# Kernel optimization log

Measured on AMD Instinct MI355X. Metric: run time of the kernel, lower is better.

The kernel has to match this reference:

```python
import jax, jax.numpy as jnp
import numpy as np

# Module hyper-parameters (match init_kwargs)
WIN = 64        # windowSize -> N
REC = 128       # receptiveSize -> M
H = 8           # numHeads
D = 32          # headDim
DIM = 256       # dim
MAXD = WIN + (REC - WIN) // 2  # maxDisparity = 96

# Static relative position index table, shape (N, M), values in [0, 2*MAXD)
_coords_x = np.arange(WIN)[:, None]
_coords_x_ = (np.arange(REC) - (REC - WIN) // 2)[None, :]
REL_IDX = jnp.asarray(_coords_x - _coords_x_ + MAXD, dtype=jnp.int32)


def setup_inputs() -> dict:
    key = jax.random.key(0)
    ks = jax.random.split(key, 12)
    B, nW = 4, 256
    B_ = B * nW
    x = jax.random.normal(ks[0], (B_, WIN, DIM), jnp.float32)
    x_ = jax.random.normal(ks[1], (B_, REC, DIM), jnp.float32)
    mask_left = jax.random.randint(ks[2], (2, WIN, REC), 0, 2, jnp.int32)
    mask_right = jax.random.randint(ks[3], (2, WIN, REC), 0, 2, jnp.int32)
    s = 0.02
    q_w = jax.random.normal(ks[4], (DIM, H * D), jnp.float32) * s
    q_b = jnp.zeros((H * D,), jnp.float32)
    kv_w = jax.random.normal(ks[5], (DIM, 2 * H * D), jnp.float32) * s
    kv_b = jnp.zeros((2 * H * D,), jnp.float32)
    proj_w = jax.random.normal(ks[6], (H * D, DIM), jnp.float32) * s
    proj_b = jnp.zeros((DIM,), jnp.float32)
    bias_table = jax.random.normal(ks[7], (2 * MAXD, H), jnp.float32) * s
    return dict(x=x, x_=x_, mask_left=mask_left, mask_right=mask_right, nW=nW,
                q_w=q_w, q_b=q_b, kv_w=kv_w, kv_b=kv_b,
                proj_w=proj_w, proj_b=proj_b, bias_table=bias_table)


def reference(x, x_, mask_left, mask_right, nW, q_w, q_b, kv_w, kv_b, proj_w, proj_b, bias_table):
    B_, N, C = x.shape
    M = x_.shape[1]
    B = B_ // nW
    scale = D ** -0.5

    q = (x @ q_w + q_b).reshape(B_, N, H, D).transpose(0, 2, 1, 3)   # b h n d
    kv = x_ @ kv_w + kv_b
    k, v = jnp.split(kv, 2, axis=-1)
    k = k.reshape(B_, M, H, D).transpose(0, 2, 1, 3)                 # b h m d
    v = v.reshape(B_, M, H, D).transpose(0, 2, 1, 3)                 # b h m d

    attn = jnp.einsum('bhnd,bhmd->bhnm', q, k) * scale
    # gathered relative position bias: (N, M, H) -> (H, N, M)
    bias = bias_table[REL_IDX].transpose(2, 0, 1)
    attn = attn + bias[None]

    mask_value = -jnp.finfo(attn.dtype).max
    attn = attn.reshape(B, nW, H, N, M)
    mc = min(mask_left.shape[0], nW)  # static python int
    ml = (mask_left[:mc] == 1)[None, :, None]        # (1, mc, 1, N, M)
    attn = attn.at[:, :mc].set(jnp.where(ml, mask_value, attn[:, :mc]))
    mr = (mask_right[mask_right.shape[0] - mc:] == 1)[None, :, None]
    attn = attn.at[:, nW - mc:].set(jnp.where(mr, mask_value, attn[:, nW - mc:]))
    attn = attn.reshape(B_, H, N, M)

    attn = jax.nn.softmax(attn, axis=-1)
    out = jnp.einsum('bhnm,bhmd->bhnd', attn, v)
    out = out.transpose(0, 2, 1, 3).reshape(B_, N, H * D)
    out = out @ proj_w + proj_b
    return out
```

## Files before the change

kernel.cpp:

```cpp
#include <hip/hip_runtime.h>
#include <float.h>


typedef __attribute__((ext_vector_type(8))) short bf16x8;
typedef __attribute__((ext_vector_type(4))) float f32x4;

static __device__ __forceinline__ unsigned int f2bf(float f) {
    unsigned int u = __float_as_uint(f);
    return (u + 0x7FFFu + ((u >> 16) & 1u)) >> 16;
}
static __device__ __forceinline__ unsigned int pack2(float lo, float hi) {
    return f2bf(lo) | (f2bf(hi) << 16);
}

__device__ unsigned short g_Wt[262144];

__global__ __launch_bounds__(256) void prep_wt(
    const float* __restrict__ q_w, const float* __restrict__ kv_w, const float* __restrict__ proj_w)
{
    const int b = blockIdx.x, k = threadIdx.x;
    float v; unsigned short* dst;
    if (b < 256)      { v = q_w[k * 256 + b];            dst = g_Wt + b * 256; }
    else if (b < 768) { v = kv_w[k * 512 + (b - 256)];   dst = g_Wt + 65536 + (b - 256) * 256; }
    else              { v = proj_w[k * 256 + (b - 768)]; dst = g_Wt + 196608 + (b - 768) * 256; }
    dst[k] = (unsigned short)f2bf(v);
}

template<int NC, int WT_OFF, bool ABF16, bool F32OUT>
__global__ __launch_bounds__(512) void gemm_mfma(
    const void* __restrict__ Ain, const float* __restrict__ bias, void* __restrict__ Cout)
{
    __shared__ __align__(16) unsigned short As[128 * 256];
    __shared__ __align__(16) unsigned short Ws[128 * 256];
    const int nbn = NC / 128;
    const int bm = blockIdx.x / nbn, bn = blockIdx.x % nbn;
    const size_t r0 = (size_t)bm * 128;
    const int c0 = bn * 128;
    const int t = threadIdx.x;
    const int wave = t >> 6, lane = t & 63;
    const int lr = lane & 15, hi = lane >> 4;
    const int rw = (wave >> 1) * 32, cw = (wave & 1) * 64;

    {
        const int row = t >> 2, a = t & 3;
        char* dst = (char*)As + row * 512;
        const int swz = (row & 7) << 4;
        if (ABF16) {
            const unsigned short* src = (const unsigned short*)Ain + (r0 + row) * 256;
            #pragma unroll
            for (int i = 0; i < 8; ++i) {
                const int k = 8 * a + 32 * i;
                const uint4 v = *(const uint4*)(src + k);
                *(uint4*)(dst + ((2 * k) ^ swz)) = v;
            }
        } else {
            const float* src = (const float*)Ain + (r0 + row) * 256;
            #pragma unroll
            for (int i = 0; i < 16; ++i) {
                const int k = 4 * a + 16 * i;
                const float4 v = *(const float4*)(src + k);
                uint2 u; u.x = pack2(v.x, v.y); u.y = pack2(v.z, v.w);
                *(uint2*)(dst + ((2 * k) ^ swz)) = u;
            }
        }
    }
    {
        const int col = t >> 2, a = t & 3;
        const unsigned short* src = g_Wt + WT_OFF + (size_t)(c0 + col) * 256;
        char* dst = (char*)Ws + col * 512;
        const int swz = (col & 7) << 4;
        #pragma unroll
        for (int i = 0; i < 8; ++i) {
            const int k = 8 * a + 32 * i;
            const uint4 v = *(const uint4*)(src + k);
            *(uint4*)(dst + ((2 * k) ^ swz)) = v;
        }
    }
    __syncthreads();

    f32x4 acc[2][4];
    #pragma unroll
    for (int ai = 0; ai < 2; ++ai)
        #pragma unroll
        for (int bj = 0; bj < 4; ++bj) acc[ai][bj] = (f32x4){0.f, 0.f, 0.f, 0.f};

    const int swzr = (lr & 7) << 4;
    #pragma unroll
    for (int kk = 0; kk < 8; ++kk) {
        const int ko = (64 * kk + 16 * hi) ^ swzr;
        bf16x8 af[2], bfr[4];
        #pragma unroll
        for (int ai = 0; ai < 2; ++ai)
            af[ai] = *(const bf16x8*)((char*)As + (rw + ai * 16 + lr) * 512 + ko);
        #pragma unroll
        for (int bj = 0; bj < 4; ++bj)
            bfr[bj] = *(const bf16x8*)((char*)Ws + (cw + bj * 16 + lr) * 512 + ko);
        #pragma unroll
        for (int ai = 0; ai < 2; ++ai)
            #pragma unroll
            for (int bj = 0; bj < 4; ++bj)
                acc[ai][bj] = __builtin_amdgcn_mfma_f32_16x16x32_bf16(af[ai], bfr[bj], acc[ai][bj], 0, 0, 0);
    }

    #pragma unroll
    for (int ai = 0; ai < 2; ++ai) {
        #pragma unroll
        for (int bj = 0; bj < 4; ++bj) {
            const int col = c0 + cw + bj * 16 + lr;
            const float bb = bias[col];
            #pragma unroll
            for (int q = 0; q < 4; ++q) {
                const size_t row = r0 + rw + ai * 16 + 4 * hi + q;
                const float val = acc[ai][bj][q] + bb;
                if (F32OUT) ((float*)Cout)[row * NC + col] = val;
                else        ((unsigned short*)Cout)[row * NC + col] = (unsigned short)f2bf(val);
            }
        }
    }
}

__global__ __launch_bounds__(256) void attn_fused(
    const unsigned short* __restrict__ qbf, const unsigned short* __restrict__ kvbf,
    const float* __restrict__ bias_table, const int* __restrict__ mask_left,
    const int* __restrict__ mask_right, unsigned short* __restrict__ aout)
{
    __shared__ __align__(16) unsigned short Qn[64 * 32];
    __shared__ __align__(16) unsigned short Kn[128 * 32];
    __shared__ __align__(16) unsigned short Vt[32 * 128];
    __shared__ __align__(16) unsigned short Pn[64 * 128];
    __shared__ float ballT[8 * 192];

    const int w = blockIdx.x;
    const int t = threadIdx.x;
    const int wave = t >> 6, lane = t & 63;
    const int lr = lane & 15, hi = lane >> 4;
    const int n0w = wave * 16;

    for (int i = t; i < 1536; i += 256) {
        const int hh = i / 192, r = i - hh * 192;
        ballT[i] = bias_table[r * 8 + hh];
    }

    const int wi = w & 255;
    const int* mbase = nullptr;
    if (wi < 2) mbase = mask_left + wi * (64 * 128);
    else if (wi >= 254) mbase = mask_right + (wi - 254) * (64 * 128);

    const float scale = 0.17677669529663687f;

    for (int h = 0; h < 8; ++h) {
        __syncthreads();
        {
            const int n = t >> 2, dq = t & 3;
            const uint4 v = *(const uint4*)(qbf + ((size_t)(w * 64 + n)) * 256 + h * 32 + dq * 8);
            *(uint4*)((char*)Qn + n * 64 + dq * 16) = v;
        }
        #pragma unroll
        for (int i = 0; i < 2; ++i) {
            const int m = (t >> 2) + 64 * i, dq = t & 3;
            const uint4 v = *(const uint4*)(kvbf + ((size_t)(w * 128 + m)) * 512 + h * 32 + dq * 8);
            *(uint4*)((char*)Kn + m * 64 + dq * 16) = v;
        }
        #pragma unroll
        for (int i = 0; i < 2; ++i) {
            const int db = (t >> 7) * 2 + i, m = t & 127;
            const uint4 v = *(const uint4*)(kvbf + ((size_t)(w * 128 + m)) * 512 + 256 + h * 32 + db * 8);
            const unsigned short* vs = (const unsigned short*)&v;
            #pragma unroll
            for (int e = 0; e < 8; ++e) {
                const int d = db * 8 + e;
                *(unsigned short*)((char*)Vt + d * 256 + ((2 * m) ^ ((d & 7) << 4))) = vs[e];
            }
        }
        __syncthreads();

        const bf16x8 qa = *(const bf16x8*)((char*)Qn + (n0w + lr) * 64 + 16 * hi);
        f32x4 sacc[8];
        #pragma unroll
        for (int mj = 0; mj < 8; ++mj) {
            sacc[mj] = (f32x4){0.f, 0.f, 0.f, 0.f};
            const bf16x8 kb = *(const bf16x8*)((char*)Kn + (mj * 16 + lr) * 64 + 16 * hi);
            sacc[mj] = __builtin_amdgcn_mfma_f32_16x16x32_bf16(qa, kb, sacc[mj], 0, 0, 0);
        }

        const float* bh = ballT + h * 192;
        #pragma unroll
        for (int mj = 0; mj < 8; ++mj) {
            const int m = 16 * mj + lr;
            #pragma unroll
            for (int q = 0; q < 4; ++q) {
                const int n = n0w + 4 * hi + q;
                sacc[mj][q] = fmaf(sacc[mj][q], scale, bh[n - m + 128]);
            }
        }
        if (mbase) {
            #pragma unroll
            for (int mj = 0; mj < 8; ++mj) {
                const int m = 16 * mj + lr;
                #pragma unroll
                for (int q = 0; q < 4; ++q) {
                    const int n = n0w + 4 * hi + q;
                    if (mbase[n * 128 + m] == 1) sacc[mj][q] = -FLT_MAX;
                }
            }
        }

        float inv[4];
        #pragma unroll
        for (int q = 0; q < 4; ++q) {
            float mx = sacc[0][q];
            #pragma unroll
            for (int mj = 1; mj < 8; ++mj) mx = fmaxf(mx, sacc[mj][q]);
            mx = fmaxf(mx, __shfl_xor(mx, 1));
            mx = fmaxf(mx, __shfl_xor(mx, 2));
            mx = fmaxf(mx, __shfl_xor(mx, 4));
            mx = fmaxf(mx, __shfl_xor(mx, 8));
            float sm = 0.f;
            #pragma unroll
            for (int mj = 0; mj < 8; ++mj) {
                sacc[mj][q] = __expf(sacc[mj][q] - mx);
                sm += sacc[mj][q];
            }
            sm += __shfl_xor(sm, 1);
            sm += __shfl_xor(sm, 2);
            sm += __shfl_xor(sm, 4);
            sm += __shfl_xor(sm, 8);
            inv[q] = 1.0f / sm;
        }

        #pragma unroll
        for (int mj = 0; mj < 8; ++mj) {
            #pragma unroll
            for (int q = 0; q < 4; ++q) {
                const float pv = sacc[mj][q];
                const float po = __shfl_xor(pv, 1);
                if (!(lane & 1)) {
                    const int n = n0w + 4 * hi + q;
                    const int m = 16 * mj + lr;
                    const unsigned int u = f2bf(pv) | (f2bf(po) << 16);
                    *(unsigned int*)((char*)Pn + n * 256 + ((2 * m) ^ ((n & 7) << 4))) = u;
                }
            }
        }

        f32x4 oacc[2];
        oacc[0] = (f32x4){0.f, 0.f, 0.f, 0.f};
        oacc[1] = (f32x4){0.f, 0.f, 0.f, 0.f};
        const int nA = n0w + lr;
        const int swzA = (nA & 7) << 4;
        #pragma unroll
        for (int kk = 0; kk < 4; ++kk) {
            const bf16x8 pa = *(const bf16x8*)((char*)Pn + nA * 256 + ((64 * kk + 16 * hi) ^ swzA));
            #pragma unroll
            for (int j = 0; j < 2; ++j) {
                const int d = j * 16 + lr;
                const bf16x8 vb = *(const bf16x8*)((char*)Vt + d * 256 + ((64 * kk + 16 * hi) ^ ((d & 7) << 4)));
                oacc[j] = __builtin_amdgcn_mfma_f32_16x16x32_bf16(pa, vb, oacc[j], 0, 0, 0);
            }
        }
        #pragma unroll
        for (int j = 0; j < 2; ++j) {
            #pragma unroll
            for (int q = 0; q < 4; ++q) {
                const int n = n0w + 4 * hi + q;
                aout[((size_t)(w * 64 + n)) * 256 + h * 32 + j * 16 + lr] =
                    (unsigned short)f2bf(oacc[j][q] * inv[q]);
            }
        }
    }
}

extern "C" void kernel_launch(void* const* d_in, const int* in_sizes, int n_in,
                              void* d_out, int out_size, void* d_ws, size_t ws_size,
                              hipStream_t stream)
{
    const float* x      = (const float*)d_in[0];
    const float* x_     = (const float*)d_in[1];
    const int*   mask_l = (const int*)d_in[2];
    const int*   mask_r = (const int*)d_in[3];
    const float* q_w    = (const float*)d_in[5];
    const float* q_b    = (const float*)d_in[6];
    const float* kv_w   = (const float*)d_in[7];
    const float* kv_b   = (const float*)d_in[8];
    const float* proj_w = (const float*)d_in[9];
    const float* proj_b = (const float*)d_in[10];
    const float* bias_t = (const float*)d_in[11];

    unsigned short* qbf  = (unsigned short*)d_ws;
    unsigned short* kvbf = qbf + (size_t)65536 * 256;
    float* out = (float*)d_out;

    prep_wt<<<1024, 256, 0, stream>>>(q_w, kv_w, proj_w);
    gemm_mfma<256, 0,      false, false><<<1024, 512, 0, stream>>>(x,  q_b,  qbf);
    gemm_mfma<512, 65536,  false, false><<<4096, 512, 0, stream>>>(x_, kv_b, kvbf);
    attn_fused<<<1024, 256, 0, stream>>>(qbf, kvbf, bias_t, mask_l, mask_r, qbf);
    gemm_mfma<256, 196608, true,  true ><<<1024, 512, 0, stream>>>(qbf, proj_b, out);
}
```

Baseline: 312.9 us.

## Give each GEMM block full output width and stream weights from global

The GEMM kernel now assigns one 128-row A tile per block and loops over every 128-column output slab inside the block. The A fragments stay in registers, and weight fragments are read directly from global memory (L2-resident) instead of being staged in shared memory. This stops the A tile from being reloaded and re-converted from fp32 for each column tile, and it halves LDS use. The cost is fewer blocks, uncoalesced per-lane global weight loads inside the MFMA loop, and 8 accumulators per wave.

```diff
diff --git a/kernel.cpp b/kernel.cpp
--- a/kernel.cpp
+++ b/kernel.cpp
@@ -27,19 +27,15 @@
 }
 
 template<int NC, int WT_OFF, bool ABF16, bool F32OUT>
-__global__ __launch_bounds__(512) void gemm_mfma(
+__global__ __launch_bounds__(512) void gemm_sa(
     const void* __restrict__ Ain, const float* __restrict__ bias, void* __restrict__ Cout)
 {
     __shared__ __align__(16) unsigned short As[128 * 256];
-    __shared__ __align__(16) unsigned short Ws[128 * 256];
-    const int nbn = NC / 128;
-    const int bm = blockIdx.x / nbn, bn = blockIdx.x % nbn;
-    const size_t r0 = (size_t)bm * 128;
-    const int c0 = bn * 128;
+    const size_t r0 = (size_t)blockIdx.x * 128;
     const int t = threadIdx.x;
     const int wave = t >> 6, lane = t & 63;
     const int lr = lane & 15, hi = lane >> 4;
-    const int rw = (wave >> 1) * 32, cw = (wave & 1) * 64;
+    const int rw = wave * 16;
 
     {
         const int row = t >> 2, a = t & 3;
@@ -64,54 +60,42 @@
             }
         }
     }
+    __syncthreads();
+
+    bf16x8 af[8];
     {
-        const int col = t >> 2, a = t & 3;
-        const unsigned short* src = g_Wt + WT_OFF + (size_t)(c0 + col) * 256;
-        char* dst = (char*)Ws + col * 512;
-        const int swz = (col & 7) << 4;
-        #pragma unroll
-        for (int i = 0; i < 8; ++i) {
-            const int k = 8 * a + 32 * i;
-            const uint4 v = *(const uint4*)(src + k);
-            *(uint4*)(dst + ((2 * k) ^ swz)) = v;
-        }
-    }
-    __syncthreads();
-
-    f32x4 acc[2][4];
+        const char* arow = (const char*)As + (rw + lr) * 512;
+        const int swzr = (lr & 7) << 4;
+        #pragma unroll
+        for (int kk = 0; kk < 8; ++kk)
+            af[kk] = *(const bf16x8*)(arow + ((64 * kk + 16 * hi) ^ swzr));
+    }
+
     #pragma unroll
-    for (int ai = 0; ai < 2; ++ai)
-        #pragma unroll
-        for (int bj = 0; bj < 4; ++bj) acc[ai][bj] = (f32x4){0.f, 0.f, 0.f, 0.f};
-
-    const int swzr = (lr & 7) << 4;
-    #pragma unroll
-    for (int kk = 0; kk < 8; ++kk) {
-        const int ko = (64 * kk + 16 * hi) ^ swzr;
-        bf16x8 af[2], bfr[4];
-        #pragma unroll
-        for (int ai = 0; ai < 2; ++ai)
-            af[ai] = *(const bf16x8*)((char*)As + (rw + ai * 16 + lr) * 512 + ko);
-        #pragma unroll
-        for (int bj = 0; bj < 4; ++bj)
-            bfr[bj] = *(const bf16x8*)((char*)Ws + (cw + bj * 16 + lr) * 512 + ko);
-        #pragma unroll
-        for (int ai = 0; ai < 2; ++ai)
-            #pragma unroll
-            for (int bj = 0; bj < 4; ++bj)
-                acc[ai][bj] = __builtin_amdgcn_mfma_f32_16x16x32_bf16(af[ai], bfr[bj], acc[ai][bj], 0, 0, 0);
-    }
-
-    #pragma unroll
-    for (int ai = 0; ai < 2; ++ai) {
-        #pragma unroll
-        for (int bj = 0; bj < 4; ++bj) {
-            const int col = c0 + cw + bj * 16 + lr;
+    for (int cs = 0; cs < NC / 128; ++cs) {
+        const int c0 = cs * 128;
+        f32x4 acc[8];
+        #pragma unroll
+        for (int bj = 0; bj < 8; ++bj) acc[bj] = (f32x4){0.f, 0.f, 0.f, 0.f};
+
+        const unsigned short* wb = g_Wt + WT_OFF + (size_t)(c0 + lr) * 256 + hi * 8;
+        #pragma unroll
+        for (int kk = 0; kk < 8; ++kk) {
+            #pragma unroll
+            for (int bj = 0; bj < 8; ++bj) {
+                const bf16x8 bfr = *(const bf16x8*)(wb + bj * (16 * 256) + kk * 32);
+                acc[bj] = __builtin_amdgcn_mfma_f32_16x16x32_bf16(af[kk], bfr, acc[bj], 0, 0, 0);
+            }
+        }
+
+        #pragma unroll
+        for (int bj = 0; bj < 8; ++bj) {
+            const int col = c0 + bj * 16 + lr;
             const float bb = bias[col];
             #pragma unroll
             for (int q = 0; q < 4; ++q) {
-                const size_t row = r0 + rw + ai * 16 + 4 * hi + q;
-                const float val = acc[ai][bj][q] + bb;
+                const size_t row = r0 + rw + 4 * hi + q;
+                const float val = acc[bj][q] + bb;
                 if (F32OUT) ((float*)Cout)[row * NC + col] = val;
                 else        ((unsigned short*)Cout)[row * NC + col] = (unsigned short)f2bf(val);
             }
@@ -291,8 +275,8 @@
     float* out = (float*)d_out;
 
     prep_wt<<<1024, 256, 0, stream>>>(q_w, kv_w, proj_w);
-    gemm_mfma<256, 0,      false, false><<<1024, 512, 0, stream>>>(x,  q_b,  qbf);
-    gemm_mfma<512, 65536,  false, false><<<4096, 512, 0, stream>>>(x_, kv_b, kvbf);
+    gemm_sa<256, 0,      false, false><<<512,  512, 0, stream>>>(x,  q_b,  qbf);
+    gemm_sa<512, 65536,  false, false><<<1024, 512, 0, stream>>>(x_, kv_b, kvbf);
     attn_fused<<<1024, 256, 0, stream>>>(qbf, kvbf, bias_t, mask_l, mask_r, qbf);
-    gemm_mfma<256, 196608, true,  true ><<<1024, 512, 0, stream>>>(qbf, proj_b, out);
-}
+    gemm_sa<256, 196608, true,  true ><<<512,  512, 0, stream>>>(qbf, proj_b, out);
+}
```

Result: slower. 524.4 us (+67.6%).
